# Kernel tuning notes

Hardware: AMD Instinct MI355X
Metric: run time of the kernel (lower is better)

Reference implementation:

```python
import jax, jax.numpy as jnp
import numpy as np

B, N1, N2, C1, C2, MLP_OUT = 16, 4096, 1024, 128, 256, 256


def setup_inputs() -> dict:
    key = jax.random.key(0)
    k = jax.random.split(key, 8)
    xyz1 = jax.random.normal(k[0], (B, N1, 3), dtype=jnp.float32)
    feat1 = jax.random.normal(k[1], (B, N1, C1), dtype=jnp.float32)
    xyz2 = jax.random.normal(k[2], (B, N2, 3), dtype=jnp.float32)
    feat2 = jax.random.normal(k[3], (B, N2, C2), dtype=jnp.float32)
    d_in = C1 + C2
    W1 = jax.random.normal(k[4], (d_in, MLP_OUT), dtype=jnp.float32) / np.sqrt(d_in)
    b1 = jnp.zeros((MLP_OUT,), dtype=jnp.float32)
    W2 = jax.random.normal(k[5], (MLP_OUT, MLP_OUT), dtype=jnp.float32) / np.sqrt(MLP_OUT)
    b2 = jnp.zeros((MLP_OUT,), dtype=jnp.float32)
    return {"xyz1": xyz1, "feat1": feat1, "xyz2": xyz2, "feat2": feat2,
            "W1": W1, "b1": b1, "W2": W2, "b2": b2}


def reference(xyz1, feat1, xyz2, feat2, W1, b1, W2, b2):
    # squared pairwise distances [B, N1, N2]
    dists = jnp.sum((xyz1[:, :, None, :] - xyz2[:, None, :, :]) ** 2, axis=-1)
    # 3 nearest neighbors (smallest distances)
    neg_d3, idx = jax.lax.top_k(-dists, 3)      # [B, N1, 3]
    d3 = jnp.maximum(-neg_d3, 1e-10)
    w = 1.0 / d3
    w = w / jnp.sum(w, axis=-1, keepdims=True)   # [B, N1, 3]
    # gather neighbor features: [B, N1, 3, C2]
    neighbor_feats = jax.vmap(lambda f, i: f[i])(feat2, idx)
    interpolated = jnp.sum(w[..., None] * neighbor_feats, axis=2)  # [B, N1, C2]
    new_feat = jnp.concatenate([interpolated, feat1], axis=-1)     # [B, N1, C2+C1]
    h = jax.nn.relu(new_feat @ W1 + b1)
    return jax.nn.relu(h @ W2 + b2)
```

## Files before the change

kernel.cpp:

```cpp
#include <hip/hip_runtime.h>
#include <cstdint>
#include <cstddef>

typedef unsigned short ushort_t;
typedef unsigned int uint_t;

typedef __bf16 bf16x8 __attribute__((ext_vector_type(8)));
typedef float floatx4 __attribute__((ext_vector_type(4)));

#define B_ 16
#define N1_ 4096
#define N2_ 1024
#define C1_ 128
#define C2_ 256
#define DIN_ 384
#define DOUT_ 256
#define M_ (B_ * N1_)


__device__ __forceinline__ ushort_t f2bf(float f) {
  unsigned int u = __builtin_bit_cast(unsigned int, f);
  u = (u + 0x7fffu + ((u >> 16) & 1u)) >> 16;
  return (ushort_t)u;
}


__global__ __launch_bounds__(256) void prep_kernel(
    const float* __restrict__ W1, const float* __restrict__ W2,
    ushort_t* __restrict__ W1s, ushort_t* __restrict__ W2s) {
  int e = blockIdx.x * 256 + threadIdx.x;
  if (e < DOUT_ * DIN_) {
    int kk = e & 31, n = (e >> 5) & 255, t = e >> 13;
    W1s[e] = f2bf(W1[(size_t)(t * 32 + kk) * DOUT_ + n]);
  }
  if (e < DOUT_ * DOUT_) {
    int kk = e & 31, n = (e >> 5) & 255, t = e >> 13;
    W2s[e] = f2bf(W2[(size_t)(t * 32 + kk) * DOUT_ + n]);
  }
}


__device__ __forceinline__ void ins_exact(float& s0, float& s1, float& s2,
                                          int& i0, int& i1, int& i2,
                                          float d, int p) {
  float ns2 = __builtin_amdgcn_fmed3f(d, s1, s2);
  float ns1 = __builtin_amdgcn_fmed3f(d, s0, s1);
  float ns0 = fminf(d, s0);
  bool c0 = d < s0, c1 = d < s1, c2 = d < s2;
  i2 = c1 ? i1 : (c2 ? p : i2);
  i1 = c0 ? i0 : (c1 ? p : i1);
  i0 = c0 ? p : i0;
  s0 = ns0; s1 = ns1; s2 = ns2;
}

__device__ __forceinline__ void ins_merge(float& s0, float& s1, float& s2,
                                          int& i0, int& i1, int& i2,
                                          float e, int j) {
  bool t0 = (e < s0) || (e == s0 && j < i0);
  bool t1 = (e < s1) || (e == s1 && j < i1);
  bool t2 = (e < s2) || (e == s2 && j < i2);
  s2 = t1 ? s1 : (t2 ? e : s2);
  i2 = t1 ? i1 : (t2 ? j : i2);
  s1 = t0 ? s0 : (t1 ? e : s1);
  i1 = t0 ? i0 : (t1 ? j : i1);
  s0 = t0 ? e : s0;
  i0 = t0 ? j : i0;
}

__global__ __launch_bounds__(256) void knn_kernel(
    const float* __restrict__ xyz1, const float* __restrict__ xyz2,
    int* __restrict__ idx_out, float* __restrict__ w_out) {
  __shared__ float4 xs4[N2_];
  int b = blockIdx.x >> 7;
  int n1base = (blockIdx.x & 127) << 5;
  const float* p2 = xyz2 + (size_t)b * N2_ * 3;
  for (int i = threadIdx.x; i < N2_; i += 256) {
    const float* s = p2 + 3 * i;
    xs4[i] = make_float4(s[0], s[1], s[2], 0.0f);
  }
  __syncthreads();

  int g = threadIdx.x >> 3;
  int sub = threadIdx.x & 7;
  int row = b * N1_ + n1base + g;
  const float* p1 = xyz1 + (size_t)row * 3;
  float x1 = p1[0], y1 = p1[1], z1 = p1[2];

  float s0 = 3.0e38f, s1 = 3.0e38f, s2 = 3.0e38f;
  int i0 = 0, i1 = 0, i2 = 0;

  int p = sub;
#pragma unroll 8
  for (int t = 0; t < N2_ / 8; ++t) {
    float4 qv = xs4[p];
    float dx = x1 - qv.x;
    float dy = y1 - qv.y;
    float dz = z1 - qv.z;
    float d = dx * dx + dy * dy + dz * dz;
    ins_exact(s0, s1, s2, i0, i1, i2, d, p);
    p += 8;
  }

#pragma unroll
  for (int mm = 1; mm <= 4; mm <<= 1) {
    float e0 = __shfl_xor(s0, mm), e1 = __shfl_xor(s1, mm), e2 = __shfl_xor(s2, mm);
    int j0 = __shfl_xor(i0, mm), j1 = __shfl_xor(i1, mm), j2 = __shfl_xor(i2, mm);
    ins_merge(s0, s1, s2, i0, i1, i2, e0, j0);
    ins_merge(s0, s1, s2, i0, i1, i2, e1, j1);
    ins_merge(s0, s1, s2, i0, i1, i2, e2, j2);
  }

  if (sub == 0) {
    float r0 = 1.0f / fmaxf(s0, 1e-10f);
    float r1 = 1.0f / fmaxf(s1, 1e-10f);
    float r2 = 1.0f / fmaxf(s2, 1e-10f);
    float s = 1.0f / (r0 + r1 + r2);
    int base = row * 3;
    idx_out[base + 0] = i0;
    idx_out[base + 1] = i1;
    idx_out[base + 2] = i2;
    w_out[base + 0] = r0 * s;
    w_out[base + 1] = r1 * s;
    w_out[base + 2] = r2 * s;
  }
}


__global__ __launch_bounds__(256, 2) void fused_kernel(
    const float* __restrict__ feat1, const float* __restrict__ feat2,
    const int* __restrict__ idx, const float* __restrict__ w,
    const ushort_t* __restrict__ W1s, const float* __restrict__ b1,
    const ushort_t* __restrict__ W2s, const float* __restrict__ b2,
    float* __restrict__ out) {
  __shared__ ushort_t As[64 * 384];
  const int tid = threadIdx.x;
  const int wave = tid >> 6;
  const int lane = tid & 63;
  const int m = lane & 15;
  const int q = lane >> 4;
  const int row0 = blockIdx.x * 64;
  const int b = row0 >> 12;

#pragma unroll 4
  for (int it = 0; it < 16; ++it) {
    int rl = wave * 16 + it;
    int row = row0 + rl;
    const int* ip = idx + (size_t)row * 3;
    const float* wp = w + (size_t)row * 3;
    int i0 = ip[0], i1 = ip[1], i2 = ip[2];
    float w0 = wp[0], w1 = wp[1], w2 = wp[2];

    const float4* f0 = (const float4*)(feat2 + ((size_t)b * N2_ + i0) * C2_);
    const float4* f1 = (const float4*)(feat2 + ((size_t)b * N2_ + i1) * C2_);
    const float4* f2 = (const float4*)(feat2 + ((size_t)b * N2_ + i2) * C2_);
    float4 a = f0[lane];
    float4 c = f1[lane];
    float4 d = f2[lane];
    float vx = w0 * a.x + w1 * c.x + w2 * d.x;
    float vy = w0 * a.y + w1 * c.y + w2 * d.y;
    float vz = w0 * a.z + w1 * c.z + w2 * d.z;
    float vw = w0 * a.w + w1 * c.w + w2 * d.w;
    uint_t lo = (uint_t)f2bf(vx) | ((uint_t)f2bf(vy) << 16);
    uint_t hi = (uint_t)f2bf(vz) | ((uint_t)f2bf(vw) << 16);
    int e = (lane >> 3) * 2048 + rl * 32 + ((4 * lane) & 31);
    *(uint2*)&As[e] = make_uint2(lo, hi);

    float2 t1 = ((const float2*)(feat1 + (size_t)row * C1_))[lane];
    uint_t pk = (uint_t)f2bf(t1.x) | ((uint_t)f2bf(t1.y) << 16);
    int e1 = (8 + (lane >> 4)) * 2048 + rl * 32 + ((2 * lane) & 31);
    *(uint_t*)&As[e1] = pk;
  }
  __syncthreads();

  const int b_off = (wave * 64 + m) * 32 + q * 8;
  const int a_base = m * 32 + q * 8;

  floatx4 acc[4][4];
#pragma unroll
  for (int i = 0; i < 4; ++i)
#pragma unroll
    for (int j = 0; j < 4; ++j) acc[i][j] = (floatx4)0.0f;

  {
    bf16x8 bf0[4], bf1[4], af[4];
#pragma unroll
    for (int j = 0; j < 4; ++j)
      bf0[j] = *(const bf16x8*)(W1s + b_off + j * 512);
#pragma unroll
    for (int t = 0; t < 12; t += 2) {
#pragma unroll
      for (int j = 0; j < 4; ++j)
        bf1[j] = *(const bf16x8*)(W1s + (size_t)(t + 1) * 8192 + b_off + j * 512);
#pragma unroll
      for (int i = 0; i < 4; ++i)
        af[i] = *(const bf16x8*)&As[t * 2048 + a_base + i * 512];
#pragma unroll
      for (int i = 0; i < 4; ++i)
#pragma unroll
        for (int j = 0; j < 4; ++j)
          acc[i][j] = __builtin_amdgcn_mfma_f32_16x16x32_bf16(af[i], bf0[j],
                                                              acc[i][j], 0, 0, 0);
      if (t + 2 < 12) {
#pragma unroll
        for (int j = 0; j < 4; ++j)
          bf0[j] = *(const bf16x8*)(W1s + (size_t)(t + 2) * 8192 + b_off + j * 512);
      }
#pragma unroll
      for (int i = 0; i < 4; ++i)
        af[i] = *(const bf16x8*)&As[(t + 1) * 2048 + a_base + i * 512];
#pragma unroll
      for (int i = 0; i < 4; ++i)
#pragma unroll
        for (int j = 0; j < 4; ++j)
          acc[i][j] = __builtin_amdgcn_mfma_f32_16x16x32_bf16(af[i], bf1[j],
                                                              acc[i][j], 0, 0, 0);
    }
  }
  __syncthreads();

  ushort_t* HS = As;
#pragma unroll
  for (int j = 0; j < 4; ++j) {
    int col = wave * 64 + j * 16 + m;
    float bv = b1[col];
    int cb = (col >> 3) & 3;
    int tb = (col >> 5) * 2048 + (col & 7);
#pragma unroll
    for (int i = 0; i < 4; ++i)
#pragma unroll
      for (int r = 0; r < 4; ++r) {
        int row = i * 16 + q * 4 + r;
        float v = acc[i][j][r] + bv;
        v = v > 0.0f ? v : 0.0f;
        int ch = cb ^ ((row >> 2) & 3);
        HS[tb + row * 32 + ch * 8] = f2bf(v);
      }
  }
  __syncthreads();

  floatx4 acc2[4][4];
#pragma unroll
  for (int i = 0; i < 4; ++i)
#pragma unroll
    for (int j = 0; j < 4; ++j) acc2[i][j] = (floatx4)0.0f;

  {
    bf16x8 bf0[4], bf1[4], af[4];
#pragma unroll
    for (int j = 0; j < 4; ++j)
      bf0[j] = *(const bf16x8*)(W2s + b_off + j * 512);
#pragma unroll
    for (int t = 0; t < 8; t += 2) {
#pragma unroll
      for (int j = 0; j < 4; ++j)
        bf1[j] = *(const bf16x8*)(W2s + (size_t)(t + 1) * 8192 + b_off + j * 512);
#pragma unroll
      for (int i = 0; i < 4; ++i) {
        int row = m + 16 * i;
        int ch = q ^ ((row >> 2) & 3);
        af[i] = *(const bf16x8*)&HS[t * 2048 + row * 32 + ch * 8];
      }
#pragma unroll
      for (int i = 0; i < 4; ++i)
#pragma unroll
        for (int j = 0; j < 4; ++j)
          acc2[i][j] = __builtin_amdgcn_mfma_f32_16x16x32_bf16(af[i], bf0[j],
                                                               acc2[i][j], 0, 0, 0);
      if (t + 2 < 8) {
#pragma unroll
        for (int j = 0; j < 4; ++j)
          bf0[j] = *(const bf16x8*)(W2s + (size_t)(t + 2) * 8192 + b_off + j * 512);
      }
#pragma unroll
      for (int i = 0; i < 4; ++i) {
        int row = m + 16 * i;
        int ch = q ^ ((row >> 2) & 3);
        af[i] = *(const bf16x8*)&HS[(t + 1) * 2048 + row * 32 + ch * 8];
      }
#pragma unroll
      for (int i = 0; i < 4; ++i)
#pragma unroll
        for (int j = 0; j < 4; ++j)
          acc2[i][j] = __builtin_amdgcn_mfma_f32_16x16x32_bf16(af[i], bf1[j],
                                                               acc2[i][j], 0, 0, 0);
    }
  }

#pragma unroll
  for (int j = 0; j < 4; ++j) {
    int col = wave * 64 + j * 16 + m;
    float bv = b2[col];
#pragma unroll
    for (int i = 0; i < 4; ++i)
#pragma unroll
      for (int r = 0; r < 4; ++r) {
        int row = i * 16 + q * 4 + r;
        float v = acc2[i][j][r] + bv;
        v = v > 0.0f ? v : 0.0f;
        out[(size_t)(row0 + row) * DOUT_ + col] = v;
      }
  }
}


constexpr size_t OFF_W1S = 0;
constexpr size_t OFF_W2S = OFF_W1S + 196608;
constexpr size_t OFF_IDX = OFF_W2S + 131072;
constexpr size_t OFF_W = OFF_IDX + 786432;
constexpr size_t WS_TOTAL = OFF_W + 786432;

extern "C" void kernel_launch(void* const* d_in, const int* in_sizes, int n_in,
                              void* d_out, int out_size, void* d_ws, size_t ws_size,
                              hipStream_t stream) {
  const float* xyz1 = (const float*)d_in[0];
  const float* feat1 = (const float*)d_in[1];
  const float* xyz2 = (const float*)d_in[2];
  const float* feat2 = (const float*)d_in[3];
  const float* W1 = (const float*)d_in[4];
  const float* b1 = (const float*)d_in[5];
  const float* W2 = (const float*)d_in[6];
  const float* b2 = (const float*)d_in[7];

  if (ws_size < WS_TOTAL) return;

  char* ws = (char*)d_ws;
  ushort_t* W1s = (ushort_t*)(ws + OFF_W1S);
  ushort_t* W2s = (ushort_t*)(ws + OFF_W2S);
  int* idx = (int*)(ws + OFF_IDX);
  float* w = (float*)(ws + OFF_W);

  prep_kernel<<<384, 256, 0, stream>>>(W1, W2, W1s, W2s);
  knn_kernel<<<B_ * (N1_ / 32), 256, 0, stream>>>(xyz1, xyz2, idx, w);
  fused_kernel<<<M_ / 64, 256, 0, stream>>>(feat1, feat2, idx, w, W1s, b1, W2s,
                                            b2, (float*)d_out);
}
```

Measured before the change: 191.0 us.

## Register-block kNN over four queries and deepen weight prefetch with swizzled A tile

The kNN kernel now has each thread track four query points, so every xyz2 value read from LDS is reused four times. Blocks shrink to 128 threads and cover 64 queries each. In the fused MLP kernel, B-fragments are prefetched four K-steps deep, and the first W1 fragments load before the gather phase to overlap it. The A tile in LDS gets an XOR swizzle to cut bank conflicts on fragment reads. The cost is more register pressure in both kernels, plus fewer kNN blocks, which may lower occupancy.

```diff
diff --git a/kernel.cpp b/kernel.cpp
--- a/kernel.cpp
+++ b/kernel.cpp
@@ -23,6 +23,9 @@
   u = (u + 0x7fffu + ((u >> 16) & 1u)) >> 16;
   return (ushort_t)u;
 }
+
+#define AS_IDX(t, row, kk) \
+  ((t) * 2048 + (row) * 32 + ((kk) ^ ((((row) >> 1) & 3) << 3)))
 
 
 __global__ __launch_bounds__(256) void prep_kernel(
@@ -67,14 +70,14 @@
   i0 = t0 ? j : i0;
 }
 
-__global__ __launch_bounds__(256) void knn_kernel(
+__global__ __launch_bounds__(128) void knn_kernel(
     const float* __restrict__ xyz1, const float* __restrict__ xyz2,
     int* __restrict__ idx_out, float* __restrict__ w_out) {
   __shared__ float4 xs4[N2_];
-  int b = blockIdx.x >> 7;
-  int n1base = (blockIdx.x & 127) << 5;
+  int b = blockIdx.x >> 6;
+  int n1base = (blockIdx.x & 63) << 6;
   const float* p2 = xyz2 + (size_t)b * N2_ * 3;
-  for (int i = threadIdx.x; i < N2_; i += 256) {
+  for (int i = threadIdx.x; i < N2_; i += 128) {
     const float* s = p2 + 3 * i;
     xs4[i] = make_float4(s[0], s[1], s[2], 0.0f);
   }
@@ -82,46 +85,60 @@
 
   int g = threadIdx.x >> 3;
   int sub = threadIdx.x & 7;
-  int row = b * N1_ + n1base + g;
-  const float* p1 = xyz1 + (size_t)row * 3;
-  float x1 = p1[0], y1 = p1[1], z1 = p1[2];
-
-  float s0 = 3.0e38f, s1 = 3.0e38f, s2 = 3.0e38f;
-  int i0 = 0, i1 = 0, i2 = 0;
+
+  float px[4], py[4], pz[4];
+  float s0[4], s1[4], s2[4];
+  int i0[4], i1[4], i2[4];
+#pragma unroll
+  for (int r = 0; r < 4; ++r) {
+    int row = b * N1_ + n1base + g + 16 * r;
+    const float* p1 = xyz1 + (size_t)row * 3;
+    px[r] = p1[0]; py[r] = p1[1]; pz[r] = p1[2];
+    s0[r] = 3.0e38f; s1[r] = 3.0e38f; s2[r] = 3.0e38f;
+    i0[r] = 0; i1[r] = 0; i2[r] = 0;
+  }
 
   int p = sub;
-#pragma unroll 8
+#pragma unroll 4
   for (int t = 0; t < N2_ / 8; ++t) {
     float4 qv = xs4[p];
-    float dx = x1 - qv.x;
-    float dy = y1 - qv.y;
-    float dz = z1 - qv.z;
-    float d = dx * dx + dy * dy + dz * dz;
-    ins_exact(s0, s1, s2, i0, i1, i2, d, p);
+#pragma unroll
+    for (int r = 0; r < 4; ++r) {
+      float dx = px[r] - qv.x, dy = py[r] - qv.y, dz = pz[r] - qv.z;
+      float d = dx * dx + dy * dy + dz * dz;
+      ins_exact(s0[r], s1[r], s2[r], i0[r], i1[r], i2[r], d, p);
+    }
     p += 8;
   }
 
 #pragma unroll
   for (int mm = 1; mm <= 4; mm <<= 1) {
-    float e0 = __shfl_xor(s0, mm), e1 = __shfl_xor(s1, mm), e2 = __shfl_xor(s2, mm);
-    int j0 = __shfl_xor(i0, mm), j1 = __shfl_xor(i1, mm), j2 = __shfl_xor(i2, mm);
-    ins_merge(s0, s1, s2, i0, i1, i2, e0, j0);
-    ins_merge(s0, s1, s2, i0, i1, i2, e1, j1);
-    ins_merge(s0, s1, s2, i0, i1, i2, e2, j2);
+#pragma unroll
+    for (int r = 0; r < 4; ++r) {
+      float e0 = __shfl_xor(s0[r], mm), e1 = __shfl_xor(s1[r], mm), e2 = __shfl_xor(s2[r], mm);
+      int j0 = __shfl_xor(i0[r], mm), j1 = __shfl_xor(i1[r], mm), j2 = __shfl_xor(i2[r], mm);
+      ins_merge(s0[r], s1[r], s2[r], i0[r], i1[r], i2[r], e0, j0);
+      ins_merge(s0[r], s1[r], s2[r], i0[r], i1[r], i2[r], e1, j1);
+      ins_merge(s0[r], s1[r], s2[r], i0[r], i1[r], i2[r], e2, j2);
+    }
   }
 
   if (sub == 0) {
-    float r0 = 1.0f / fmaxf(s0, 1e-10f);
-    float r1 = 1.0f / fmaxf(s1, 1e-10f);
-    float r2 = 1.0f / fmaxf(s2, 1e-10f);
-    float s = 1.0f / (r0 + r1 + r2);
-    int base = row * 3;
-    idx_out[base + 0] = i0;
-    idx_out[base + 1] = i1;
-    idx_out[base + 2] = i2;
-    w_out[base + 0] = r0 * s;
-    w_out[base + 1] = r1 * s;
-    w_out[base + 2] = r2 * s;
+#pragma unroll
+    for (int r = 0; r < 4; ++r) {
+      int row = b * N1_ + n1base + g + 16 * r;
+      float r0 = 1.0f / fmaxf(s0[r], 1e-10f);
+      float r1 = 1.0f / fmaxf(s1[r], 1e-10f);
+      float r2 = 1.0f / fmaxf(s2[r], 1e-10f);
+      float s = 1.0f / (r0 + r1 + r2);
+      int base = row * 3;
+      idx_out[base + 0] = i0[r];
+      idx_out[base + 1] = i1[r];
+      idx_out[base + 2] = i2[r];
+      w_out[base + 0] = r0 * s;
+      w_out[base + 1] = r1 * s;
+      w_out[base + 2] = r2 * s;
+    }
   }
 }
 
@@ -141,6 +158,16 @@
   const int row0 = blockIdx.x * 64;
   const int b = row0 >> 12;
 
+  const int b_off = (wave * 64 + m) * 32 + q * 8;
+
+  bf16x8 w0[4], w1[4], w2[4], w3[4], af[4];
+
+#pragma unroll
+  for (int j = 0; j < 4; ++j) {
+    w0[j] = *(const bf16x8*)(W1s + b_off + j * 512);
+    w1[j] = *(const bf16x8*)(W1s + 8192 + b_off + j * 512);
+  }
+
 #pragma unroll 4
   for (int it = 0; it < 16; ++it) {
     int rl = wave * 16 + it;
@@ -148,7 +175,7 @@
     const int* ip = idx + (size_t)row * 3;
     const float* wp = w + (size_t)row * 3;
     int i0 = ip[0], i1 = ip[1], i2 = ip[2];
-    float w0 = wp[0], w1 = wp[1], w2 = wp[2];
+    float w0v = wp[0], w1v = wp[1], w2v = wp[2];
 
     const float4* f0 = (const float4*)(feat2 + ((size_t)b * N2_ + i0) * C2_);
     const float4* f1 = (const float4*)(feat2 + ((size_t)b * N2_ + i1) * C2_);
@@ -156,65 +183,84 @@
     float4 a = f0[lane];
     float4 c = f1[lane];
     float4 d = f2[lane];
-    float vx = w0 * a.x + w1 * c.x + w2 * d.x;
-    float vy = w0 * a.y + w1 * c.y + w2 * d.y;
-    float vz = w0 * a.z + w1 * c.z + w2 * d.z;
-    float vw = w0 * a.w + w1 * c.w + w2 * d.w;
+    float vx = w0v * a.x + w1v * c.x + w2v * d.x;
+    float vy = w0v * a.y + w1v * c.y + w2v * d.y;
+    float vz = w0v * a.z + w1v * c.z + w2v * d.z;
+    float vw = w0v * a.w + w1v * c.w + w2v * d.w;
     uint_t lo = (uint_t)f2bf(vx) | ((uint_t)f2bf(vy) << 16);
     uint_t hi = (uint_t)f2bf(vz) | ((uint_t)f2bf(vw) << 16);
-    int e = (lane >> 3) * 2048 + rl * 32 + ((4 * lane) & 31);
+    int e = AS_IDX(lane >> 3, rl, (4 * lane) & 31);
     *(uint2*)&As[e] = make_uint2(lo, hi);
 
     float2 t1 = ((const float2*)(feat1 + (size_t)row * C1_))[lane];
     uint_t pk = (uint_t)f2bf(t1.x) | ((uint_t)f2bf(t1.y) << 16);
-    int e1 = (8 + (lane >> 4)) * 2048 + rl * 32 + ((2 * lane) & 31);
+    int e1 = AS_IDX(8 + (lane >> 4), rl, (2 * lane) & 31);
     *(uint_t*)&As[e1] = pk;
   }
   __syncthreads();
 
-  const int b_off = (wave * 64 + m) * 32 + q * 8;
-  const int a_base = m * 32 + q * 8;
-
   floatx4 acc[4][4];
 #pragma unroll
   for (int i = 0; i < 4; ++i)
 #pragma unroll
     for (int j = 0; j < 4; ++j) acc[i][j] = (floatx4)0.0f;
 
-  {
-    bf16x8 bf0[4], bf1[4], af[4];
-#pragma unroll
-    for (int j = 0; j < 4; ++j)
-      bf0[j] = *(const bf16x8*)(W1s + b_off + j * 512);
-#pragma unroll
-    for (int t = 0; t < 12; t += 2) {
-#pragma unroll
-      for (int j = 0; j < 4; ++j)
-        bf1[j] = *(const bf16x8*)(W1s + (size_t)(t + 1) * 8192 + b_off + j * 512);
-#pragma unroll
-      for (int i = 0; i < 4; ++i)
-        af[i] = *(const bf16x8*)&As[t * 2048 + a_base + i * 512];
-#pragma unroll
-      for (int i = 0; i < 4; ++i)
-#pragma unroll
-        for (int j = 0; j < 4; ++j)
-          acc[i][j] = __builtin_amdgcn_mfma_f32_16x16x32_bf16(af[i], bf0[j],
-                                                              acc[i][j], 0, 0, 0);
-      if (t + 2 < 12) {
-#pragma unroll
-        for (int j = 0; j < 4; ++j)
-          bf0[j] = *(const bf16x8*)(W1s + (size_t)(t + 2) * 8192 + b_off + j * 512);
+#pragma unroll
+  for (int tt = 0; tt < 12; tt += 4) {
+#pragma unroll
+    for (int j = 0; j < 4; ++j) {
+      w2[j] = *(const bf16x8*)(W1s + (size_t)(tt + 2) * 8192 + b_off + j * 512);
+      w3[j] = *(const bf16x8*)(W1s + (size_t)(tt + 3) * 8192 + b_off + j * 512);
+    }
+#pragma unroll
+    for (int i = 0; i < 4; ++i)
+      af[i] = *(const bf16x8*)&As[AS_IDX(tt, m + 16 * i, q * 8)];
+#pragma unroll
+    for (int i = 0; i < 4; ++i)
+#pragma unroll
+      for (int j = 0; j < 4; ++j)
+        acc[i][j] = __builtin_amdgcn_mfma_f32_16x16x32_bf16(af[i], w0[j],
+                                                            acc[i][j], 0, 0, 0);
+#pragma unroll
+    for (int i = 0; i < 4; ++i)
+      af[i] = *(const bf16x8*)&As[AS_IDX(tt + 1, m + 16 * i, q * 8)];
+#pragma unroll
+    for (int i = 0; i < 4; ++i)
+#pragma unroll
+      for (int j = 0; j < 4; ++j)
+        acc[i][j] = __builtin_amdgcn_mfma_f32_16x16x32_bf16(af[i], w1[j],
+                                                            acc[i][j], 0, 0, 0);
+    if (tt + 4 < 12) {
+#pragma unroll
+      for (int j = 0; j < 4; ++j) {
+        w0[j] = *(const bf16x8*)(W1s + (size_t)(tt + 4) * 8192 + b_off + j * 512);
+        w1[j] = *(const bf16x8*)(W1s + (size_t)(tt + 5) * 8192 + b_off + j * 512);
       }
-#pragma unroll
-      for (int i = 0; i < 4; ++i)
-        af[i] = *(const bf16x8*)&As[(t + 1) * 2048 + a_base + i * 512];
-#pragma unroll
-      for (int i = 0; i < 4; ++i)
-#pragma unroll
-        for (int j = 0; j < 4; ++j)
-          acc[i][j] = __builtin_amdgcn_mfma_f32_16x16x32_bf16(af[i], bf1[j],
-                                                              acc[i][j], 0, 0, 0);
-    }
+    }
+#pragma unroll
+    for (int i = 0; i < 4; ++i)
+      af[i] = *(const bf16x8*)&As[AS_IDX(tt + 2, m + 16 * i, q * 8)];
+#pragma unroll
+    for (int i = 0; i < 4; ++i)
+#pragma unroll
+      for (int j = 0; j < 4; ++j)
+        acc[i][j] = __builtin_amdgcn_mfma_f32_16x16x32_bf16(af[i], w2[j],
+                                                            acc[i][j], 0, 0, 0);
+#pragma unroll
+    for (int i = 0; i < 4; ++i)
+      af[i] = *(const bf16x8*)&As[AS_IDX(tt + 3, m + 16 * i, q * 8)];
+#pragma unroll
+    for (int i = 0; i < 4; ++i)
+#pragma unroll
+      for (int j = 0; j < 4; ++j)
+        acc[i][j] = __builtin_amdgcn_mfma_f32_16x16x32_bf16(af[i], w3[j],
+                                                            acc[i][j], 0, 0, 0);
+  }
+
+#pragma unroll
+  for (int j = 0; j < 4; ++j) {
+    w0[j] = *(const bf16x8*)(W2s + b_off + j * 512);
+    w1[j] = *(const bf16x8*)(W2s + 8192 + b_off + j * 512);
   }
   __syncthreads();
 
@@ -244,46 +290,68 @@
 #pragma unroll
     for (int j = 0; j < 4; ++j) acc2[i][j] = (floatx4)0.0f;
 
-  {
-    bf16x8 bf0[4], bf1[4], af[4];
-#pragma unroll
-    for (int j = 0; j < 4; ++j)
-      bf0[j] = *(const bf16x8*)(W2s + b_off + j * 512);
-#pragma unroll
-    for (int t = 0; t < 8; t += 2) {
-#pragma unroll
-      for (int j = 0; j < 4; ++j)
-        bf1[j] = *(const bf16x8*)(W2s + (size_t)(t + 1) * 8192 + b_off + j * 512);
-#pragma unroll
-      for (int i = 0; i < 4; ++i) {
-        int row = m + 16 * i;
-        int ch = q ^ ((row >> 2) & 3);
-        af[i] = *(const bf16x8*)&HS[t * 2048 + row * 32 + ch * 8];
+#pragma unroll
+  for (int tt = 0; tt < 8; tt += 4) {
+#pragma unroll
+    for (int j = 0; j < 4; ++j) {
+      w2[j] = *(const bf16x8*)(W2s + (size_t)(tt + 2) * 8192 + b_off + j * 512);
+      w3[j] = *(const bf16x8*)(W2s + (size_t)(tt + 3) * 8192 + b_off + j * 512);
+    }
+#pragma unroll
+    for (int i = 0; i < 4; ++i) {
+      int row = m + 16 * i;
+      int ch = q ^ ((row >> 2) & 3);
+      af[i] = *(const bf16x8*)&HS[tt * 2048 + row * 32 + ch * 8];
+    }
+#pragma unroll
+    for (int i = 0; i < 4; ++i)
+#pragma unroll
+      for (int j = 0; j < 4; ++j)
+        acc2[i][j] = __builtin_amdgcn_mfma_f32_16x16x32_bf16(af[i], w0[j],
+                                                             acc2[i][j], 0, 0, 0);
+#pragma unroll
+    for (int i = 0; i < 4; ++i) {
+      int row = m + 16 * i;
+      int ch = q ^ ((row >> 2) & 3);
+      af[i] = *(const bf16x8*)&HS[(tt + 1) * 2048 + row * 32 + ch * 8];
+    }
+#pragma unroll
+    for (int i = 0; i < 4; ++i)
+#pragma unroll
+      for (int j = 0; j < 4; ++j)
+        acc2[i][j] = __builtin_amdgcn_mfma_f32_16x16x32_bf16(af[i], w1[j],
+                                                             acc2[i][j], 0, 0, 0);
+    if (tt + 4 < 8) {
+#pragma unroll
+      for (int j = 0; j < 4; ++j) {
+        w0[j] = *(const bf16x8*)(W2s + (size_t)(tt + 4) * 8192 + b_off + j * 512);
+        w1[j] = *(const bf16x8*)(W2s + (size_t)(tt + 5) * 8192 + b_off + j * 512);
       }
-#pragma unroll
-      for (int i = 0; i < 4; ++i)
-#pragma unroll
-        for (int j = 0; j < 4; ++j)
-          acc2[i][j] = __builtin_amdgcn_mfma_f32_16x16x32_bf16(af[i], bf0[j],
-                                                               acc2[i][j], 0, 0, 0);
-      if (t + 2 < 8) {
-#pragma unroll
-        for (int j = 0; j < 4; ++j)
-          bf0[j] = *(const bf16x8*)(W2s + (size_t)(t + 2) * 8192 + b_off + j * 512);
-      }
-#pragma unroll
-      for (int i = 0; i < 4; ++i) {
-        int row = m + 16 * i;
-        int ch = q ^ ((row >> 2) & 3);
-        af[i] = *(const bf16x8*)&HS[(t + 1) * 2048 + row * 32 + ch * 8];
-      }
-#pragma unroll
-      for (int i = 0; i < 4; ++i)
-#pragma unroll
-        for (int j = 0; j < 4; ++j)
-          acc2[i][j] = __builtin_amdgcn_mfma_f32_16x16x32_bf16(af[i], bf1[j],
-                                                               acc2[i][j], 0, 0, 0);
-    }
+    }
+#pragma unroll
+    for (int i = 0; i < 4; ++i) {
+      int row = m + 16 * i;
+      int ch = q ^ ((row >> 2) & 3);
+      af[i] = *(const bf16x8*)&HS[(tt + 2) * 2048 + row * 32 + ch * 8];
+    }
+#pragma unroll
+    for (int i = 0; i < 4; ++i)
+#pragma unroll
+      for (int j = 0; j < 4; ++j)
+        acc2[i][j] = __builtin_amdgcn_mfma_f32_16x16x32_bf16(af[i], w2[j],
+                                                             acc2[i][j], 0, 0, 0);
+#pragma unroll
+    for (int i = 0; i < 4; ++i) {
+      int row = m + 16 * i;
+      int ch = q ^ ((row >> 2) & 3);
+      af[i] = *(const bf16x8*)&HS[(tt + 3) * 2048 + row * 32 + ch * 8];
+    }
+#pragma unroll
+    for (int i = 0; i < 4; ++i)
+#pragma unroll
+      for (int j = 0; j < 4; ++j)
+        acc2[i][j] = __builtin_amdgcn_mfma_f32_16x16x32_bf16(af[i], w3[j],
+                                                             acc2[i][j], 0, 0, 0);
   }
 
 #pragma unroll
@@ -330,7 +398,7 @@
   float* w = (float*)(ws + OFF_W);
 
   prep_kernel<<<384, 256, 0, stream>>>(W1, W2, W1s, W2s);
-  knn_kernel<<<B_ * (N1_ / 32), 256, 0, stream>>>(xyz1, xyz2, idx, w);
+  knn_kernel<<<B_ * (N1_ / 64), 128, 0, stream>>>(xyz1, xyz2, idx, w);
   fused_kernel<<<M_ / 64, 256, 0, stream>>>(feat1, feat2, idx, w, W1s, b1, W2s,
                                             b2, (float*)d_out);
 }
```

Result: slower. 217.6 us (+13.9%).
